# Kernel optimization log

Measured on AMD Instinct MI355X. Metric: run time of the kernel, lower is better.

## Reference

```python
import jax, jax.numpy as jnp
import numpy as np

B, S, D = 2, 400, 512  # batch, seq (src == tgt for self-attention), dim; attn_hidden=0 so d == D


def setup_inputs() -> dict:
    key = jax.random.key(0)
    ks = jax.random.split(key, 9)
    inv = 1.0 / np.sqrt(D)
    return {
        "input": jax.random.normal(ks[0], (B, S, D), jnp.float32),
        "memory_bank": jax.random.normal(ks[1], (B, S, D), jnp.float32),
        # lengths in [S//2, S], guaranteed >= 2 so no row is fully masked
        "memory_lengths": jax.random.randint(ks[2], (B,), S // 2, S + 1, jnp.int32),
        "Wq": jax.random.normal(ks[3], (D, D), jnp.float32) * inv,   # linear_query.weight^T
        "bq": jax.random.normal(ks[4], (D,), jnp.float32) * inv,      # linear_query.bias
        "Wc": jax.random.normal(ks[5], (D, D), jnp.float32) * inv,   # linear_context.weight^T
        "v": jax.random.normal(ks[6], (D,), jnp.float32) * inv,       # v.weight (d -> 1)
        "Wout": jax.random.normal(ks[7], (2 * D, D), jnp.float32) * inv,  # linear_out.weight^T
        "bout": jax.random.normal(ks[8], (D,), jnp.float32) * inv,
    }


def reference(input, memory_bank, memory_lengths, Wq, bq, Wc, v, Wout, bout):
    b, s, d = memory_bank.shape
    # Bahdanau/mlp score: v^T tanh(Wq q + b + Wc h)
    wq = jnp.einsum("btd,de->bte", input, Wq) + bq            # [B,T,d]
    uh = jnp.einsum("bsd,de->bse", memory_bank, Wc)           # [B,S,d]
    wquh = jnp.tanh(wq[:, :, None, :] + uh[:, None, :, :])    # [B,T,S,d] big intermediate
    scores = jnp.einsum("btse,e->bts", wquh, v)               # [B,T,S]
    # padding mask (j < length) with self position masked out on the diagonal
    pos = jnp.arange(s)
    key_mask = pos[None, :] < memory_lengths[:, None]         # [B,S]
    mask = key_mask[:, None, :] & (pos[:, None] != pos[None, :])  # [B,T,S]
    scores = jnp.where(mask, scores, -jnp.inf)
    align = jax.nn.softmax(scores, axis=2)                    # [B,T,S]
    c = jnp.einsum("bts,bsd->btd", align, memory_bank)        # context [B,T,D]
    concat_c = jnp.concatenate([c, input], axis=2)            # [B,T,2D]
    attn_h = jnp.einsum("btf,fd->btd", concat_c, Wout) + bout # [B,T,D]
    # mlp variant: no sigmoid gating
    return attn_h.transpose(1, 0, 2), align.transpose(1, 0, 2)  # [T,B,D], [T,B,S]
```

## Files before the change

kernel.cpp:

```cpp
#include <hip/hip_runtime.h>
#include <math.h>

#define BB 2
#define SS 400
#define DD 512
#define TWO_LOG2E 2.8853900817779268f

#if __has_builtin(__builtin_amdgcn_exp2f)
#define EXP2F(x) __builtin_amdgcn_exp2f(x)
#else
#define EXP2F(x) exp2f(x)
#endif
#define RCPF(x) __builtin_amdgcn_rcpf(x)

#define EAOFF 0
#define MOFF 409600
#define EB4OFF 819200
#define XOFF 1228800

typedef __bf16 bf16x8 __attribute__((ext_vector_type(8)));
typedef float floatx16 __attribute__((ext_vector_type(16)));

__global__ __launch_bounds__(256) void k0_all(
    const float* __restrict__ Wq, const float* __restrict__ Wc,
    const float* __restrict__ Wout, const float* __restrict__ input,
    const float* __restrict__ mbk, unsigned short* __restrict__ wt,
    unsigned short* __restrict__ ahi, unsigned short* __restrict__ alo)
{
    const int gid = blockIdx.x;
    if (gid < 1024) {
        const int g   = gid >> 9;
        const int rem = gid & 511;
        const int k0  = (rem & 15) * 32;
        const int n0  = (rem >> 4) * 32;

        __shared__ float tile[32][33];
        const int nn  = threadIdx.x & 31;
        const int kk0 = threadIdx.x >> 5;
        const int n   = n0 + nn;

        #pragma unroll
        for (int p = 0; p < 4; ++p) {
            const int k = k0 + kk0 + p * 8;
            float val;
            if (n0 < 512) val = (g ? Wc : Wq)[(size_t)k * 512 + n];
            else          val = Wout[((size_t)(g ? k : 512 + k)) * 512 + (n - 512)];
            tile[kk0 + p * 8][nn] = val;
        }
        __syncthreads();

        const int kc = threadIdx.x & 31;
        #pragma unroll
        for (int p = 0; p < 4; ++p) {
            const int nl = (threadIdx.x >> 5) + p * 8;
            const __bf16 h = (__bf16)tile[kc][nl];
            wt[((size_t)(g * 1024 + n0 + nl)) * 512 + k0 + kc] =
                __builtin_bit_cast(unsigned short, h);
        }
    } else {
        const int cid = gid - 1024;
        const int g   = (cid >= 400) ? 1 : 0;
        const int i4  = (cid - g * 400) * 256 + threadIdx.x;
        const float4 a = ((const float4*)(g ? mbk : input))[i4];
        ushort4 h, l;
        #pragma unroll
        for (int j = 0; j < 4; ++j) {
            const float av = (&a.x)[j];
            const __bf16 hh = (__bf16)av;
            (&h.x)[j] = __builtin_bit_cast(unsigned short, hh);
            const __bf16 ll = (__bf16)(av - (float)hh);
            (&l.x)[j] = __builtin_bit_cast(unsigned short, ll);
        }
        ((ushort4*)(ahi + (size_t)g * 409600))[i4] = h;
        ((ushort4*)(alo + (size_t)g * 409600))[i4] = l;
    }
}

__global__ __launch_bounds__(64) void k1_mfma(
    const unsigned short* __restrict__ ahi, const unsigned short* __restrict__ alo,
    const unsigned short* __restrict__ wt, const float* __restrict__ bq,
    const float* __restrict__ bout, float* __restrict__ ws,
    float* __restrict__ out0)
{
    const int lane = threadIdx.x;
    const int mt   = blockIdx.x;
    const int np   = blockIdx.y;
    const int g    = blockIdx.z;
    const int m    = lane & 31;
    const int kh   = lane >> 5;
    const int n0   = np * 64;

    const size_t arow = ((size_t)g * 800 + mt * 32 + m) * 512 + kh * 8;
    const unsigned short* __restrict__ ah = ahi + arow;
    const unsigned short* __restrict__ al = alo + arow;
    const unsigned short* __restrict__ w0 =
        wt + ((size_t)(g * 1024 + n0 + m)) * 512 + kh * 8;
    const unsigned short* __restrict__ w1 = w0 + (size_t)32 * 512;

    floatx16 acc0h, acc0l, acc1h, acc1l;
    #pragma unroll
    for (int i = 0; i < 16; ++i) { acc0h[i] = 0.f; acc0l[i] = 0.f;
                                   acc1h[i] = 0.f; acc1l[i] = 0.f; }

    #pragma unroll 4
    for (int ks = 0; ks < 32; ++ks) {
        const bf16x8 va0 = *(const bf16x8*)(ah + ks * 16);
        const bf16x8 va1 = *(const bf16x8*)(al + ks * 16);
        const bf16x8 bh0 = *(const bf16x8*)(w0 + ks * 16);
        const bf16x8 bh1 = *(const bf16x8*)(w1 + ks * 16);

        acc0h = __builtin_amdgcn_mfma_f32_32x32x16_bf16(va0, bh0, acc0h, 0, 0, 0);
        acc0l = __builtin_amdgcn_mfma_f32_32x32x16_bf16(va1, bh0, acc0l, 0, 0, 0);
        acc1h = __builtin_amdgcn_mfma_f32_32x32x16_bf16(va0, bh1, acc1h, 0, 0, 0);
        acc1l = __builtin_amdgcn_mfma_f32_32x32x16_bf16(va1, bh1, acc1l, 0, 0, 0);
    }

    const floatx16 c0 = acc0h + acc0l;
    const floatx16 c1 = acc1h + acc1l;
    const int rbase = kh * 4;

    #pragma unroll
    for (int r = 0; r < 16; ++r) {
        const int row  = (r & 3) + 8 * (r >> 2) + rbase;
        const int grow = mt * 32 + row;
        const int bi   = (grow >= SS) ? 1 : 0;
        const int rl   = grow - bi * SS;
        #pragma unroll
        for (int u = 0; u < 2; ++u) {
            const float val  = u ? c1[r] : c0[r];
            const int   gcol = n0 + u * 32 + m;
            if (g == 0) {
                if (gcol < 512) {
                    ws[EAOFF + (size_t)grow * 512 + gcol] =
                        EXP2F(TWO_LOG2E * (val + bq[gcol]));
                } else {
                    const int d = gcol - 512;
                    out0[((size_t)(rl * BB + bi)) * 512 + d] = val + bout[d];
                }
            } else {
                if (gcol < 512) {
                    ws[EB4OFF + (size_t)((bi * 128 + (gcol >> 2)) * SS + rl) * 4
                       + (gcol & 3)] = EXP2F(TWO_LOG2E * val);
                } else {
                    ws[MOFF + (size_t)grow * 512 + (gcol - 512)] = val;
                }
            }
        }
    }
}

__global__ __launch_bounds__(448) void k2_attn(
    const float* __restrict__ ws, const float* __restrict__ v,
    const int* __restrict__ lens, float* __restrict__ out1)
{
    const int tp = blockIdx.x;
    const int b  = blockIdx.y;
    const int t0 = tp * 2;
    const int t1 = t0 + 1;
    const int tid = threadIdx.x;
    const int s   = tid;
    const int sidx = (s < SS) ? s : 0;
    const int len  = lens[b];

    __shared__ float lea[2][512];
    __shared__ float lv[512];
    for (int i = tid; i < 1024; i += 448)
        lea[i >> 9][i & 511] =
            ws[EAOFF + (size_t)(b * SS + t0 + (i >> 9)) * 512 + (i & 511)];
    for (int i = tid; i < 512; i += 448) lv[i] = v[i];
    __syncthreads();

    const float4* __restrict__ eb4 =
        (const float4*)(ws + EB4OFF) + (size_t)b * 128 * SS + sidx;

    float acc0 = 0.f, acc1 = 0.f;
    #pragma unroll 4
    for (int e4 = 0; e4 < 128; ++e4) {
        const float4 eb  = eb4[(size_t)e4 * SS];
        const float4 vv  = *(const float4*)&lv[e4 * 4];
        const float4 ea0 = *(const float4*)&lea[0][e4 * 4];
        const float4 ea1 = *(const float4*)&lea[1][e4 * 4];
        #pragma unroll
        for (int j = 0; j < 4; ++j) {
            const float ebv = (&eb.x)[j];
            const float vj  = (&vv.x)[j];
            acc0 = fmaf(vj, RCPF(fmaf((&ea0.x)[j], ebv, 1.f)), acc0);
            acc1 = fmaf(vj, RCPF(fmaf((&ea1.x)[j], ebv, 1.f)), acc1);
        }
    }

    const bool v0 = (s < SS) && (s < len) && (s != t0);
    const bool v1 = (s < SS) && (s < len) && (s != t1);
    const float sc0 = v0 ? -2.f * acc0 : -INFINITY;
    const float sc1 = v1 ? -2.f * acc1 : -INFINITY;

    __shared__ float wred0[8], wred1[8];
    const int wid  = tid >> 6;
    const int lane = tid & 63;

    float m0 = sc0, m1 = sc1;
    #pragma unroll
    for (int off = 32; off > 0; off >>= 1) {
        m0 = fmaxf(m0, __shfl_xor(m0, off));
        m1 = fmaxf(m1, __shfl_xor(m1, off));
    }
    if (lane == 0) { wred0[wid] = m0; wred1[wid] = m1; }
    __syncthreads();
    float mx0 = wred0[0], mx1 = wred1[0];
    #pragma unroll
    for (int w = 1; w < 7; ++w) {
        mx0 = fmaxf(mx0, wred0[w]);
        mx1 = fmaxf(mx1, wred1[w]);
    }
    __syncthreads();

    const float p0 = v0 ? __expf(sc0 - mx0) : 0.f;
    const float p1 = v1 ? __expf(sc1 - mx1) : 0.f;
    float s0v = p0, s1v = p1;
    #pragma unroll
    for (int off = 32; off > 0; off >>= 1) {
        s0v += __shfl_xor(s0v, off);
        s1v += __shfl_xor(s1v, off);
    }
    if (lane == 0) { wred0[wid] = s0v; wred1[wid] = s1v; }
    __syncthreads();
    float tot0 = wred0[0], tot1 = wred1[0];
    #pragma unroll
    for (int w = 1; w < 7; ++w) { tot0 += wred0[w]; tot1 += wred1[w]; }
    const float inv0 = RCPF(tot0);
    const float inv1 = RCPF(tot1);

    if (s < SS) {
        out1[((size_t)(t0 * BB) + b) * SS + s] = p0 * inv0;
        out1[((size_t)(t1 * BB) + b) * SS + s] = p1 * inv1;
    }
}

__global__ __launch_bounds__(256) void k3_out(
    const float* __restrict__ ws, const float* __restrict__ align_out,
    float* __restrict__ out0)
{
    const int d     = blockIdx.x * 256 + threadIdx.x;
    const int r0    = blockIdx.y * 4;
    const int s0    = blockIdx.z * 200;
    const int b     = (r0 >= SS) ? 1 : 0;
    const int tbase = r0 - b * SS;

    const float* __restrict__ Mb = ws + MOFF + (size_t)b * SS * DD;

    float acc[4];
    #pragma unroll
    for (int j = 0; j < 4; ++j) acc[j] = 0.f;

    float mA[4], mB[4];
    float4 alA[4], alB[4];

    auto LOAD = [&](float (&mm)[4], float4 (&al)[4], int s) {
        #pragma unroll
        for (int i = 0; i < 4; ++i)
            mm[i] = Mb[(size_t)(s + i) * DD + d];
        #pragma unroll
        for (int j = 0; j < 4; ++j)
            al[j] = *(const float4*)(align_out +
                     ((size_t)((tbase + j) * BB) + b) * SS + s);
    };
    auto FMA4 = [&](const float (&mm)[4], const float4 (&al)[4]) {
        #pragma unroll
        for (int j = 0; j < 4; ++j) {
            acc[j] = fmaf(al[j].x, mm[0], acc[j]);
            acc[j] = fmaf(al[j].y, mm[1], acc[j]);
            acc[j] = fmaf(al[j].z, mm[2], acc[j]);
            acc[j] = fmaf(al[j].w, mm[3], acc[j]);
        }
    };

    LOAD(mA, alA, s0);
    for (int s = s0; s < s0 + 200; s += 8) {
        LOAD(mB, alB, s + 4);
        FMA4(mA, alA);
        if (s + 8 < s0 + 200) LOAD(mA, alA, s + 8);
        FMA4(mB, alB);
    }

    #pragma unroll
    for (int j = 0; j < 4; ++j)
        unsafeAtomicAdd(&out0[((size_t)((tbase + j) * BB) + b) * DD + d], acc[j]);
}

extern "C" void kernel_launch(void* const* d_in, const int* in_sizes, int n_in,
                              void* d_out, int out_size, void* d_ws, size_t ws_size,
                              hipStream_t stream)
{
    const float* input = (const float*)d_in[0];
    const float* mbk   = (const float*)d_in[1];
    const int*   lens  = (const int*)d_in[2];
    const float* Wq    = (const float*)d_in[3];
    const float* bq    = (const float*)d_in[4];
    const float* Wc    = (const float*)d_in[5];
    const float* v     = (const float*)d_in[6];
    const float* Wout  = (const float*)d_in[7];
    const float* bout  = (const float*)d_in[8];

    float* out0 = (float*)d_out;
    float* out1 = out0 + (size_t)BB * SS * DD;
    float* ws   = (float*)d_ws;
    unsigned short* x16 = (unsigned short*)(ws + XOFF);
    unsigned short* wt  = x16;
    unsigned short* ahi = x16 + 1048576;
    unsigned short* alo = ahi + 819200;

    hipLaunchKernelGGL(k0_all, dim3(1824), dim3(256), 0, stream,
                       Wq, Wc, Wout, input, mbk, wt, ahi, alo);
    hipLaunchKernelGGL(k1_mfma, dim3(25, 16, 2), dim3(64), 0, stream,
                       ahi, alo, wt, bq, bout, ws, out0);
    hipLaunchKernelGGL(k2_attn, dim3(200, 2), dim3(448), 0, stream,
                       ws, v, lens, out1);
    hipLaunchKernelGGL(k3_out, dim3(2, 200, 2), dim3(256), 0, stream,
                       ws, out1, out0);
}
```

Before: 154.3 us.

## Fuse context-weighted sum into attention kernel and drop separate output kernel

The attention kernel now runs 512 threads per block and keeps the normalized alignment rows in shared memory. It then computes the context vector c = align·M for its two query rows directly, adding into out0 without atomics. This removes the k3_out launch and the global re-read of the alignment, at the cost of each block streaming the whole per-batch M matrix (400x512) with only two rows of reuse. That means far less reuse per M load than the old 4-row tiled kernel, and the extra 64 threads do no useful work in the score phase.

```diff
diff --git a/kernel.cpp b/kernel.cpp
--- a/kernel.cpp
+++ b/kernel.cpp
@@ -149,9 +149,10 @@
     }
 }
 
-__global__ __launch_bounds__(448) void k2_attn(
+__global__ __launch_bounds__(512) void k2_attn(
     const float* __restrict__ ws, const float* __restrict__ v,
-    const int* __restrict__ lens, float* __restrict__ out1)
+    const int* __restrict__ lens, float* __restrict__ out1,
+    float* __restrict__ out0)
 {
     const int tp = blockIdx.x;
     const int b  = blockIdx.y;
@@ -164,10 +165,12 @@
 
     __shared__ float lea[2][512];
     __shared__ float lv[512];
-    for (int i = tid; i < 1024; i += 448)
-        lea[i >> 9][i & 511] =
-            ws[EAOFF + (size_t)(b * SS + t0 + (i >> 9)) * 512 + (i & 511)];
-    for (int i = tid; i < 512; i += 448) lv[i] = v[i];
+    __shared__ float lal[SS][2];
+    __shared__ float wred0[8], wred1[8];
+
+    lv[tid] = v[tid];
+    lea[0][tid] = ws[EAOFF + (size_t)(b * SS + t0) * 512 + tid];
+    lea[1][tid] = ws[EAOFF + (size_t)(b * SS + t1) * 512 + tid];
     __syncthreads();
 
     const float4* __restrict__ eb4 =
@@ -194,7 +197,6 @@
     const float sc0 = v0 ? -2.f * acc0 : -INFINITY;
     const float sc1 = v1 ? -2.f * acc1 : -INFINITY;
 
-    __shared__ float wred0[8], wred1[8];
     const int wid  = tid >> 6;
     const int lane = tid & 63;
 
@@ -208,7 +210,7 @@
     __syncthreads();
     float mx0 = wred0[0], mx1 = wred1[0];
     #pragma unroll
-    for (int w = 1; w < 7; ++w) {
+    for (int w = 1; w < 8; ++w) {
         mx0 = fmaxf(mx0, wred0[w]);
         mx1 = fmaxf(mx1, wred1[w]);
     }
@@ -226,65 +228,38 @@
     __syncthreads();
     float tot0 = wred0[0], tot1 = wred1[0];
     #pragma unroll
-    for (int w = 1; w < 7; ++w) { tot0 += wred0[w]; tot1 += wred1[w]; }
+    for (int w = 1; w < 8; ++w) { tot0 += wred0[w]; tot1 += wred1[w]; }
     const float inv0 = RCPF(tot0);
     const float inv1 = RCPF(tot1);
 
     if (s < SS) {
-        out1[((size_t)(t0 * BB) + b) * SS + s] = p0 * inv0;
-        out1[((size_t)(t1 * BB) + b) * SS + s] = p1 * inv1;
-    }
-}
-
-__global__ __launch_bounds__(256) void k3_out(
-    const float* __restrict__ ws, const float* __restrict__ align_out,
-    float* __restrict__ out0)
-{
-    const int d     = blockIdx.x * 256 + threadIdx.x;
-    const int r0    = blockIdx.y * 4;
-    const int s0    = blockIdx.z * 200;
-    const int b     = (r0 >= SS) ? 1 : 0;
-    const int tbase = r0 - b * SS;
+        const float a0 = p0 * inv0;
+        const float a1 = p1 * inv1;
+        out1[((size_t)(t0 * BB) + b) * SS + s] = a0;
+        out1[((size_t)(t1 * BB) + b) * SS + s] = a1;
+        lal[s][0] = a0;
+        lal[s][1] = a1;
+    }
+    __syncthreads();
 
     const float* __restrict__ Mb = ws + MOFF + (size_t)b * SS * DD;
-
-    float acc[4];
-    #pragma unroll
-    for (int j = 0; j < 4; ++j) acc[j] = 0.f;
-
-    float mA[4], mB[4];
-    float4 alA[4], alB[4];
-
-    auto LOAD = [&](float (&mm)[4], float4 (&al)[4], int s) {
-        #pragma unroll
-        for (int i = 0; i < 4; ++i)
-            mm[i] = Mb[(size_t)(s + i) * DD + d];
-        #pragma unroll
-        for (int j = 0; j < 4; ++j)
-            al[j] = *(const float4*)(align_out +
-                     ((size_t)((tbase + j) * BB) + b) * SS + s);
-    };
-    auto FMA4 = [&](const float (&mm)[4], const float4 (&al)[4]) {
-        #pragma unroll
-        for (int j = 0; j < 4; ++j) {
-            acc[j] = fmaf(al[j].x, mm[0], acc[j]);
-            acc[j] = fmaf(al[j].y, mm[1], acc[j]);
-            acc[j] = fmaf(al[j].z, mm[2], acc[j]);
-            acc[j] = fmaf(al[j].w, mm[3], acc[j]);
-        }
-    };
-
-    LOAD(mA, alA, s0);
-    for (int s = s0; s < s0 + 200; s += 8) {
-        LOAD(mB, alB, s + 4);
-        FMA4(mA, alA);
-        if (s + 8 < s0 + 200) LOAD(mA, alA, s + 8);
-        FMA4(mB, alB);
-    }
-
-    #pragma unroll
-    for (int j = 0; j < 4; ++j)
-        unsafeAtomicAdd(&out0[((size_t)((tbase + j) * BB) + b) * DD + d], acc[j]);
+    const int d = tid;
+    float c0a = 0.f, c0b = 0.f, c1a = 0.f, c1b = 0.f;
+    #pragma unroll 4
+    for (int sp = 0; sp < SS; sp += 2) {
+        const float mv0 = Mb[(size_t)sp * DD + d];
+        const float mv1 = Mb[(size_t)(sp + 1) * DD + d];
+        const float2 a0 = *(const float2*)&lal[sp][0];
+        const float2 a1 = *(const float2*)&lal[sp + 1][0];
+        c0a = fmaf(a0.x, mv0, c0a);
+        c1a = fmaf(a0.y, mv0, c1a);
+        c0b = fmaf(a1.x, mv1, c0b);
+        c1b = fmaf(a1.y, mv1, c1b);
+    }
+    const size_t o0 = ((size_t)(t0 * BB) + b) * DD + d;
+    const size_t o1 = ((size_t)(t1 * BB) + b) * DD + d;
+    out0[o0] += c0a + c0b;
+    out0[o1] += c1a + c1b;
 }
 
 extern "C" void kernel_launch(void* const* d_in, const int* in_sizes, int n_in,
@@ -313,8 +288,6 @@
                        Wq, Wc, Wout, input, mbk, wt, ahi, alo);
     hipLaunchKernelGGL(k1_mfma, dim3(25, 16, 2), dim3(64), 0, stream,
                        ahi, alo, wt, bq, bout, ws, out0);
-    hipLaunchKernelGGL(k2_attn, dim3(200, 2), dim3(448), 0, stream,
-                       ws, v, lens, out1);
-    hipLaunchKernelGGL(k3_out, dim3(2, 200, 2), dim3(256), 0, stream,
-                       ws, out1, out0);
-}
+    hipLaunchKernelGGL(k2_attn, dim3(200, 2), dim3(512), 0, stream,
+                       ws, v, lens, out1, out0);
+}
```

New measurement: 146.1 us. 1.06x faster.
